# Kernel optimization log

Measured on AMD Instinct MI355X. Metric: run time of the kernel, lower is better.

The kernel has to match this reference:

```python
import jax, jax.numpy as jnp
import numpy as np

VOCAB, EMBD, H1, H2, OUT = 100000, 128, 256, 128, 1
EPS = 1e-12

def _layernorm(x, g, b):
    mu = jnp.mean(x, axis=-1, keepdims=True)
    var = jnp.mean(jnp.square(x - mu), axis=-1, keepdims=True)
    return (x - mu) * jax.lax.rsqrt(var + EPS) * g + b

def setup_inputs() -> dict:
    key = jax.random.key(0)
    ks = jax.random.split(key, 10)
    B, S = 4096, 50
    return {
        "entity_ids": jax.random.randint(ks[0], (B, S), 0, VOCAB),
        "entity_length": jax.random.randint(ks[1], (B,), 0, S + 1),
        "emb_table": jax.random.normal(ks[2], (VOCAB, EMBD), jnp.float32),
        "ln1_g": jnp.ones((EMBD,), jnp.float32),
        "ln1_b": jnp.zeros((EMBD,), jnp.float32),
        "w1": jax.random.normal(ks[3], (EMBD, H1), jnp.float32) * (1.0 / np.sqrt(EMBD)),
        "b1": jnp.zeros((H1,), jnp.float32),
        "w2": jax.random.normal(ks[4], (H1, H2), jnp.float32) * (1.0 / np.sqrt(H1)),
        "b2": jnp.zeros((H2,), jnp.float32),
        "ln2_g": jnp.ones((H2,), jnp.float32),
        "ln2_b": jnp.zeros((H2,), jnp.float32),
        "fc_w": jax.random.normal(ks[5], (H2, OUT), jnp.float32) * (1.0 / np.sqrt(H2)),
        "fc_b": jnp.zeros((OUT,), jnp.float32),
    }

def reference(entity_ids, entity_length, emb_table, ln1_g, ln1_b, w1, b1, w2, b2, ln2_g, ln2_b, fc_w, fc_b):
    # embed: [B, S, EMBD]
    x = emb_table[entity_ids]
    x = _layernorm(x, ln1_g, ln1_b)
    # MLP (dropout is identity in eval); torch GELU default is exact erf form
    x = jax.nn.gelu(x @ w1 + b1, approximate=False) @ w2 + b2  # [B, S, H2]
    # ragged max-pool over first length positions (length 0 treated as 1)
    lengths = jnp.maximum(entity_length, 1)  # [B]
    S = x.shape[1]
    mask = jnp.arange(S)[None, :] < lengths[:, None]  # [B, S]
    x = jnp.max(jnp.where(mask[:, :, None], x, -jnp.inf), axis=1)  # [B, H2]
    x = _layernorm(x, ln2_g, ln2_b)
    return (x @ fc_w + fc_b).squeeze(-1)  # [B]
```

## Files before the change

### kernel.cpp

```cpp
#include <hip/hip_runtime.h>
#include <hip/hip_bf16.h>
#include <math.h>

typedef __attribute__((ext_vector_type(8))) _Float16 half8;
typedef __attribute__((ext_vector_type(4))) float f32x4;

#define EMBD 128
#define H1 256
#define H2 128
#define SLEN 50

__device__ __forceinline__ float gelu_exact(float h) {
    float ah = fabsf(h);
    float d  = fmaf(0.23163845f, ah, 1.0f);
    float t;
    asm("v_rcp_f32 %0, %1" : "=v"(t) : "v"(d));
    float p = fmaf(1.061405429f, t, -1.453152027f);
    p = fmaf(p, t, 1.421413741f);
    p = fmaf(p, t, -0.284496736f);
    p = fmaf(p, t, 0.254829592f);
    p = p * t;
    float e;
    float x2 = h * h * -0.72134752f;
    asm("v_exp_f32 %0, %1" : "=v"(e) : "v"(x2));
    float er = fmaf(-p, e, 1.0f);
    return fmaf(0.5f * ah, er, 0.5f * h);
}

#define BARRIER_LDS() asm volatile("s_waitcnt lgkmcnt(0)\n\ts_barrier" ::: "memory")

__global__ __launch_bounds__(256) void prep_weights(
    const float* __restrict__ w1, const float* __restrict__ w2,
    half8* __restrict__ ws)
{
    int f = blockIdx.x * 256 + threadIdx.x;
    half8 v;
    if (f < 4096) {
        int lane = f & 63;
        int nt = (f >> 6) & 3, kt = (f >> 8) & 3, w = (f >> 10) & 3;
        int col = w * 64 + nt * 16 + (lane & 15);
        int kb  = kt * 32 + (lane >> 4) * 8;
        #pragma unroll
        for (int i = 0; i < 8; ++i) v[i] = (_Float16)w1[(size_t)(kb + i) * H1 + col];
        ws[f] = v;
    } else {
        int f2 = f - 4096;
        int lane = f2 & 63;
        int nt = (f2 >> 6) & 1, kt = (f2 >> 7) & 7, w = (f2 >> 10) & 3;
        int col = w * 32 + nt * 16 + (lane & 15);
        int kb  = kt * 32 + (lane >> 4) * 8;
        #pragma unroll
        for (int i = 0; i < 8; ++i) v[i] = (_Float16)w2[(size_t)(kb + i) * H2 + col];
        ws[4096 + f2] = v;
    }
}

__global__ __launch_bounds__(256, 2) void entity_encoder_kernel(
    const int* __restrict__ ids, const int* __restrict__ lens,
    const float* __restrict__ emb, const float* __restrict__ ln1g,
    const float* __restrict__ ln1b, const float* __restrict__ b1,
    const float* __restrict__ b2, const float* __restrict__ ln2g,
    const float* __restrict__ ln2b, const float* __restrict__ fcw,
    const float* __restrict__ fcb, const half8* __restrict__ wfrag,
    float* __restrict__ out)
{
    const int tid = threadIdx.x;
    const int w  = tid >> 6;
    const int l  = tid & 63;
    const int ln = l & 15;
    const int lg = l >> 4;
    const int g16 = w * 4 + lg;

    __shared__ __align__(16) _Float16 x_lds[32][EMBD + 8];
    __shared__ __align__(16) _Float16 h1_lds[32][H1 + 8];
    __shared__ float pool_lds[2][H2];

    half8 w1f[4][4];
    #pragma unroll
    for (int kt = 0; kt < 4; ++kt)
      #pragma unroll
      for (int nt = 0; nt < 4; ++nt)
        w1f[kt][nt] = wfrag[((w * 4 + kt) * 4 + nt) * 64 + l];
    half8 w2f[8][2];
    #pragma unroll
    for (int kt = 0; kt < 8; ++kt)
      #pragma unroll
      for (int nt = 0; nt < 2; ++nt)
        w2f[kt][nt] = wfrag[4096 + ((w * 8 + kt) * 2 + nt) * 64 + l];

    float g1r[8], b1r[8];
    #pragma unroll
    for (int i = 0; i < 8; ++i) { g1r[i] = ln1g[ln * 8 + i]; b1r[i] = ln1b[ln * 8 + i]; }
    float b1v[4];
    #pragma unroll
    for (int nt = 0; nt < 4; ++nt) b1v[nt] = b1[w * 64 + nt * 16 + ln];
    float b2v[2];
    #pragma unroll
    for (int nt = 0; nt < 2; ++nt) b2v[nt] = b2[w * 32 + nt * 16 + ln];
    float g2a = ln2g[l], g2c = ln2g[l + 64];
    float b2a = ln2b[l], b2c = ln2b[l + 64];
    float fwa = fcw[l],  fwc = fcw[l + 64];
    float fcb0 = fcb[0];

    int rows[4], Ts[4];
    #pragma unroll
    for (int i = 0; i < 4; ++i) {
        rows[i] = blockIdx.x + i * (int)gridDim.x;
        int T = lens[rows[i]];
        Ts[i] = T < 1 ? 1 : (T > SLEN ? SLEN : T);
    }

    float4 pa0[2], pa1[2]; bool va[2];
    #pragma unroll
    for (int s = 0; s < 2; ++s) {
        va[s] = (g16 < Ts[s]);
        if (va[s]) {
            int id = ids[rows[s] * SLEN + g16];
            const float4* src = (const float4*)(emb + (size_t)id * EMBD + ln * 8);
            pa0[s] = src[0]; pa1[s] = src[1];
        }
    }

    for (int j = 0; j < 2; ++j) {
        const int TA = Ts[2 * j], TB = Ts[2 * j + 1];
        const int ntA = (TA + 15) >> 4, ntB = (TB + 15) >> 4;
        const int ntiles = ntA > ntB ? ntA : ntB;
        float poolr[2][2];
        #pragma unroll
        for (int m = 0; m < 2; ++m) { poolr[m][0] = -INFINITY; poolr[m][1] = -INFINITY; }

        for (int mt = 0; mt < ntiles; ++mt) {
            #pragma unroll
            for (int s = 0; s < 2; ++s) {
                half8 xo;
                if (va[s]) {
                    float v[8] = {pa0[s].x, pa0[s].y, pa0[s].z, pa0[s].w,
                                  pa1[s].x, pa1[s].y, pa1[s].z, pa1[s].w};
                    float sm = 0.f, ss = 0.f;
                    #pragma unroll
                    for (int k = 0; k < 8; ++k) { sm += v[k]; ss += v[k] * v[k]; }
                    #pragma unroll
                    for (int m = 1; m < 16; m <<= 1) {
                        sm += __shfl_xor(sm, m, 64);
                        ss += __shfl_xor(ss, m, 64);
                    }
                    float mu  = sm * (1.f / 128.f);
                    float var = ss * (1.f / 128.f) - mu * mu;
                    float rs  = rsqrtf(var + 1e-12f);
                    #pragma unroll
                    for (int k = 0; k < 8; ++k)
                        xo[k] = (_Float16)((v[k] - mu) * rs * g1r[k] + b1r[k]);
                } else {
                    #pragma unroll
                    for (int k = 0; k < 8; ++k) xo[k] = (_Float16)0.f;
                }
                *(half8*)&x_lds[s * 16 + g16][ln * 8] = xo;
            }

            float4 pb0[2], pb1[2]; bool vb[2] = {false, false};
            {
                int nj = j, nmt = mt + 1;
                if (nmt >= ntiles) { nj = j + 1; nmt = 0; }
                if (nj < 2) {
                    #pragma unroll
                    for (int s = 0; s < 2; ++s) {
                        int tn = nmt * 16 + g16;
                        if (tn < Ts[2 * nj + s]) {
                            vb[s] = true;
                            int id = ids[rows[2 * nj + s] * SLEN + tn];
                            const float4* src = (const float4*)(emb + (size_t)id * EMBD + ln * 8);
                            pb0[s] = src[0]; pb1[s] = src[1];
                        }
                    }
                }
            }

            BARRIER_LDS();

            f32x4 acc[2][4];
            #pragma unroll
            for (int m = 0; m < 2; ++m)
              #pragma unroll
              for (int nt = 0; nt < 4; ++nt) acc[m][nt] = (f32x4){0,0,0,0};
            #pragma unroll
            for (int kt = 0; kt < 4; ++kt) {
                half8 a0 = *(const half8*)&x_lds[ln][kt * 32 + lg * 8];
                half8 a1 = *(const half8*)&x_lds[16 + ln][kt * 32 + lg * 8];
                #pragma unroll
                for (int nt = 0; nt < 4; ++nt) {
                    acc[0][nt] = __builtin_amdgcn_mfma_f32_16x16x32_f16(a0, w1f[kt][nt], acc[0][nt], 0, 0, 0);
                    acc[1][nt] = __builtin_amdgcn_mfma_f32_16x16x32_f16(a1, w1f[kt][nt], acc[1][nt], 0, 0, 0);
                }
            }
            #pragma unroll
            for (int m = 0; m < 2; ++m)
              #pragma unroll
              for (int nt = 0; nt < 4; ++nt) {
                int col = w * 64 + nt * 16 + ln;
                #pragma unroll
                for (int g2 = 0; g2 < 4; ++g2) {
                    int row = m * 16 + lg * 4 + g2;
                    float h = acc[m][nt][g2] + b1v[nt];
                    h1_lds[row][col] = (_Float16)gelu_exact(h);
                }
              }

            BARRIER_LDS();

            f32x4 acc2[2][2];
            #pragma unroll
            for (int m = 0; m < 2; ++m) { acc2[m][0] = (f32x4){0,0,0,0}; acc2[m][1] = (f32x4){0,0,0,0}; }
            #pragma unroll
            for (int kt = 0; kt < 8; ++kt) {
                half8 a0 = *(const half8*)&h1_lds[ln][kt * 32 + lg * 8];
                half8 a1 = *(const half8*)&h1_lds[16 + ln][kt * 32 + lg * 8];
                #pragma unroll
                for (int nt = 0; nt < 2; ++nt) {
                    acc2[0][nt] = __builtin_amdgcn_mfma_f32_16x16x32_f16(a0, w2f[kt][nt], acc2[0][nt], 0, 0, 0);
                    acc2[1][nt] = __builtin_amdgcn_mfma_f32_16x16x32_f16(a1, w2f[kt][nt], acc2[1][nt], 0, 0, 0);
                }
            }
            #pragma unroll
            for (int m = 0; m < 2; ++m) {
                const int Tm = m ? TB : TA;
                #pragma unroll
                for (int nt = 0; nt < 2; ++nt) {
                    float tm = -INFINITY;
                    #pragma unroll
                    for (int g2 = 0; g2 < 4; ++g2) {
                        int trow = lg * 4 + g2;
                        bool valid = (mt * 16 + trow) < Tm;
                        float h = acc2[m][nt][g2] + b2v[nt];
                        if (valid) tm = fmaxf(tm, h);
                    }
                    tm = fmaxf(tm, __shfl_xor(tm, 16, 64));
                    tm = fmaxf(tm, __shfl_xor(tm, 32, 64));
                    poolr[m][nt] = fmaxf(poolr[m][nt], tm);
                }
            }

            #pragma unroll
            for (int s = 0; s < 2; ++s) {
                if (vb[s]) { pa0[s] = pb0[s]; pa1[s] = pb1[s]; }
                va[s] = vb[s];
            }
        }

        if (lg == 0) {
            #pragma unroll
            for (int m = 0; m < 2; ++m)
              #pragma unroll
              for (int nt = 0; nt < 2; ++nt)
                pool_lds[m][w * 32 + nt * 16 + ln] = poolr[m][nt];
        }
        BARRIER_LDS();

        if (w < 2) {
            float v0 = pool_lds[w][l], v1 = pool_lds[w][l + 64];
            float s = v0 + v1, ss = v0 * v0 + v1 * v1;
            #pragma unroll
            for (int m = 1; m < 64; m <<= 1) {
                s  += __shfl_xor(s,  m, 64);
                ss += __shfl_xor(ss, m, 64);
            }
            float mu  = s * (1.f / 128.f);
            float var = ss * (1.f / 128.f) - mu * mu;
            float rs  = rsqrtf(var + 1e-12f);
            float n0 = (v0 - mu) * rs * g2a + b2a;
            float n1 = (v1 - mu) * rs * g2c + b2c;
            float dot = n0 * fwa + n1 * fwc;
            #pragma unroll
            for (int m = 1; m < 64; m <<= 1) dot += __shfl_xor(dot, m, 64);
            if (l == 0) out[rows[2 * j + w]] = dot + fcb0;
        }
        BARRIER_LDS();
    }
}

extern "C" void kernel_launch(void* const* d_in, const int* in_sizes, int n_in,
                              void* d_out, int out_size, void* d_ws, size_t ws_size,
                              hipStream_t stream) {
    const int*   ids  = (const int*)d_in[0];
    const int*   lens = (const int*)d_in[1];
    const float* emb  = (const float*)d_in[2];
    const float* ln1g = (const float*)d_in[3];
    const float* ln1b = (const float*)d_in[4];
    const float* w1   = (const float*)d_in[5];
    const float* b1   = (const float*)d_in[6];
    const float* w2   = (const float*)d_in[7];
    const float* b2   = (const float*)d_in[8];
    const float* ln2g = (const float*)d_in[9];
    const float* ln2b = (const float*)d_in[10];
    const float* fcw  = (const float*)d_in[11];
    const float* fcb  = (const float*)d_in[12];
    float* out = (float*)d_out;
    half8* ws = (half8*)d_ws;

    hipLaunchKernelGGL(prep_weights, dim3(32), dim3(256), 0, stream, w1, w2, ws);

    int nblocks = out_size / 4;
    hipLaunchKernelGGL(entity_encoder_kernel, dim3(nblocks), dim3(256), 0, stream,
                       ids, lens, emb, ln1g, ln1b, b1, b2, ln2g, ln2b, fcw, fcb,
                       ws, out);
}
```

Measured before the change: 79.86 us.

## Compact valid tokens into dense tiles and pool via segmented max with partials

Replaces the per-row padded tiling with a compaction pass that packs only the valid tokens (id plus row tag) into a dense stream. A persistent dense kernel processes full 32-token tiles, and a head kernel finishes the pooling and the final layernorm/fc. The aim is to remove wasted MFMA work on padding in partially filled 16-token tiles and to balance load across blocks. In exchange it adds three kernel launches, an atomic prefix step, a large partial-buffer initialisation, and segmented-max bookkeeping that relies on a row spanning at most three tiles.

```diff
diff --git a/kernel.cpp b/kernel.cpp
--- a/kernel.cpp
+++ b/kernel.cpp
@@ -3,12 +3,23 @@
 #include <math.h>
 
 typedef __attribute__((ext_vector_type(8))) _Float16 half8;
+typedef __attribute__((ext_vector_type(4))) _Float16 half4;
 typedef __attribute__((ext_vector_type(4))) float f32x4;
 
 #define EMBD 128
 #define H1 256
 #define H2 128
 #define SLEN 50
+#define NROWS 4096
+#define MAXTOK (NROWS * SLEN)
+#define MTILE 32
+#define MAXTILES ((MAXTOK + MTILE - 1) / MTILE)
+#define DENSE_GRID 1024
+
+#define WS_FRAGS   0
+#define WS_CNT     131072
+#define WS_PACKED  131200
+#define WS_PARTIAL 950400
 
 __device__ __forceinline__ float gelu_exact(float h) {
     float ah = fabsf(h);
@@ -29,40 +40,73 @@
 
 #define BARRIER_LDS() asm volatile("s_waitcnt lgkmcnt(0)\n\ts_barrier" ::: "memory")
 
-__global__ __launch_bounds__(256) void prep_weights(
+__global__ __launch_bounds__(256) void prep_kernel(
     const float* __restrict__ w1, const float* __restrict__ w2,
-    half8* __restrict__ ws)
+    half8* __restrict__ frags, int* __restrict__ cnt,
+    float* __restrict__ partial)
 {
-    int f = blockIdx.x * 256 + threadIdx.x;
-    half8 v;
-    if (f < 4096) {
-        int lane = f & 63;
-        int nt = (f >> 6) & 3, kt = (f >> 8) & 3, w = (f >> 10) & 3;
-        int col = w * 64 + nt * 16 + (lane & 15);
-        int kb  = kt * 32 + (lane >> 4) * 8;
-        #pragma unroll
-        for (int i = 0; i < 8; ++i) v[i] = (_Float16)w1[(size_t)(kb + i) * H1 + col];
-        ws[f] = v;
+    int b = blockIdx.x, t = threadIdx.x;
+    if (b < 32) {
+        int f = b * 256 + t;
+        half8 v;
+        if (f < 4096) {
+            int lane = f & 63;
+            int nt = (f >> 6) & 3, kt = (f >> 8) & 3, w = (f >> 10) & 3;
+            int col = w * 64 + nt * 16 + (lane & 15);
+            int kb  = kt * 32 + (lane >> 4) * 8;
+            #pragma unroll
+            for (int i = 0; i < 8; ++i) v[i] = (_Float16)w1[(size_t)(kb + i) * H1 + col];
+            frags[f] = v;
+        } else {
+            int f2 = f - 4096;
+            int lane = f2 & 63;
+            int nt = (f2 >> 6) & 1, kt = (f2 >> 7) & 7, w = (f2 >> 10) & 3;
+            int col = w * 32 + nt * 16 + (lane & 15);
+            int kb  = kt * 32 + (lane >> 4) * 8;
+            #pragma unroll
+            for (int i = 0; i < 8; ++i) v[i] = (_Float16)w2[(size_t)(kb + i) * H2 + col];
+            frags[4096 + f2] = v;
+        }
+    } else if (b == 32) {
+        if (t == 0) *cnt = 0;
     } else {
-        int f2 = f - 4096;
-        int lane = f2 & 63;
-        int nt = (f2 >> 6) & 1, kt = (f2 >> 7) & 7, w = (f2 >> 10) & 3;
-        int col = w * 32 + nt * 16 + (lane & 15);
-        int kb  = kt * 32 + (lane >> 4) * 8;
-        #pragma unroll
-        for (int i = 0; i < 8; ++i) v[i] = (_Float16)w2[(size_t)(kb + i) * H2 + col];
-        ws[4096 + f2] = v;
+        int idx = (b - 33) * 256 + t;
+        if (idx < NROWS * 256) {
+            int r = idx >> 8, rem = idx & 255;
+            partial[(size_t)r * 384 + 128 + rem] = -INFINITY;
+        }
     }
 }
 
-__global__ __launch_bounds__(256, 2) void entity_encoder_kernel(
+__global__ __launch_bounds__(256) void compact_kernel(
     const int* __restrict__ ids, const int* __restrict__ lens,
+    unsigned* __restrict__ packed, int* __restrict__ cnt)
+{
+    int gtid = blockIdx.x * 256 + threadIdx.x;
+    int lane = threadIdx.x & 63;
+    int len = lens[gtid]; len = len < 1 ? 1 : (len > SLEN ? SLEN : len);
+    int inc = len;
+    #pragma unroll
+    for (int off = 1; off < 64; off <<= 1) {
+        int v = __shfl_up(inc, off, 64);
+        if (lane >= off) inc += v;
+    }
+    int wave_total = __shfl(inc, 63, 64);
+    int wbase;
+    if (lane == 0) wbase = atomicAdd(cnt, wave_total);
+    wbase = __shfl(wbase, 0, 64);
+    int base = wbase + inc - len;
+    unsigned rtag = (unsigned)gtid << 17;
+    for (int t = 0; t < len; ++t)
+        packed[base + t] = (unsigned)ids[gtid * SLEN + t] | rtag;
+}
+
+__global__ __launch_bounds__(256) void dense_kernel(
+    const unsigned* __restrict__ packed, const int* __restrict__ cnt,
     const float* __restrict__ emb, const float* __restrict__ ln1g,
     const float* __restrict__ ln1b, const float* __restrict__ b1,
-    const float* __restrict__ b2, const float* __restrict__ ln2g,
-    const float* __restrict__ ln2b, const float* __restrict__ fcw,
-    const float* __restrict__ fcb, const half8* __restrict__ wfrag,
-    float* __restrict__ out)
+    const float* __restrict__ b2, const half8* __restrict__ wfrag,
+    float* __restrict__ partial)
 {
     const int tid = threadIdx.x;
     const int w  = tid >> 6;
@@ -71,9 +115,9 @@
     const int lg = l >> 4;
     const int g16 = w * 4 + lg;
 
-    __shared__ __align__(16) _Float16 x_lds[32][EMBD + 8];
-    __shared__ __align__(16) _Float16 h1_lds[32][H1 + 8];
-    __shared__ float pool_lds[2][H2];
+    __shared__ __align__(16) _Float16 x_lds[MTILE][EMBD + 8];
+    __shared__ __align__(16) _Float16 h1_lds[MTILE][H1 + 8];
+    __shared__ unsigned tok_lds[MTILE + 2];
 
     half8 w1f[4][4];
     #pragma unroll
@@ -91,190 +135,182 @@
     float g1r[8], b1r[8];
     #pragma unroll
     for (int i = 0; i < 8; ++i) { g1r[i] = ln1g[ln * 8 + i]; b1r[i] = ln1b[ln * 8 + i]; }
-    float b1v[4];
-    #pragma unroll
-    for (int nt = 0; nt < 4; ++nt) b1v[nt] = b1[w * 64 + nt * 16 + ln];
+    f32x4 b1tv[4];
+    #pragma unroll
+    for (int nt = 0; nt < 4; ++nt)
+        b1tv[nt] = *(const f32x4*)&b1[w * 64 + nt * 16 + lg * 4];
     float b2v[2];
     #pragma unroll
     for (int nt = 0; nt < 2; ++nt) b2v[nt] = b2[w * 32 + nt * 16 + ln];
+
+    const int total = *cnt;
+
+    for (int tile = blockIdx.x; tile * MTILE < total; tile += gridDim.x) {
+        const int base = tile * MTILE;
+
+        if (tid < MTILE) {
+            unsigned pk = 0xFFFFFFFFu;
+            if (base + tid < total) pk = packed[base + tid];
+            tok_lds[tid] = pk;
+        } else if (tid == MTILE) {
+            tok_lds[MTILE] = (base > 0) ? packed[base - 1] : 0xFFFFFFFFu;
+        }
+
+        #pragma unroll
+        for (int s = 0; s < 2; ++s) {
+            int tl = s * 16 + g16;
+            int gidx = base + tl;
+            half8 xo;
+            if (gidx < total) {
+                unsigned pk = packed[gidx];
+                int id = (int)(pk & 0x1FFFFu);
+                const float4* src = (const float4*)(emb + (size_t)id * EMBD + ln * 8);
+                float4 p0 = src[0], p1 = src[1];
+                float v[8] = {p0.x, p0.y, p0.z, p0.w, p1.x, p1.y, p1.z, p1.w};
+                float sm = 0.f, ss = 0.f;
+                #pragma unroll
+                for (int k = 0; k < 8; ++k) { sm += v[k]; ss += v[k] * v[k]; }
+                #pragma unroll
+                for (int m = 1; m < 16; m <<= 1) {
+                    sm += __shfl_xor(sm, m, 64);
+                    ss += __shfl_xor(ss, m, 64);
+                }
+                float mu  = sm * (1.f / 128.f);
+                float var = ss * (1.f / 128.f) - mu * mu;
+                float rs  = rsqrtf(var + 1e-12f);
+                #pragma unroll
+                for (int k = 0; k < 8; ++k)
+                    xo[k] = (_Float16)((v[k] - mu) * rs * g1r[k] + b1r[k]);
+            } else {
+                #pragma unroll
+                for (int k = 0; k < 8; ++k) xo[k] = (_Float16)0.f;
+            }
+            *(half8*)&x_lds[tl][ln * 8] = xo;
+        }
+
+        BARRIER_LDS();
+
+        f32x4 acc[2][4];
+        #pragma unroll
+        for (int m = 0; m < 2; ++m)
+          #pragma unroll
+          for (int nt = 0; nt < 4; ++nt) acc[m][nt] = (f32x4){0,0,0,0};
+        #pragma unroll
+        for (int kt = 0; kt < 4; ++kt) {
+            half8 bf0 = *(const half8*)&x_lds[ln][kt * 32 + lg * 8];
+            half8 bf1 = *(const half8*)&x_lds[16 + ln][kt * 32 + lg * 8];
+            #pragma unroll
+            for (int nt = 0; nt < 4; ++nt) {
+                acc[0][nt] = __builtin_amdgcn_mfma_f32_16x16x32_f16(w1f[kt][nt], bf0, acc[0][nt], 0, 0, 0);
+                acc[1][nt] = __builtin_amdgcn_mfma_f32_16x16x32_f16(w1f[kt][nt], bf1, acc[1][nt], 0, 0, 0);
+            }
+        }
+        #pragma unroll
+        for (int m = 0; m < 2; ++m)
+          #pragma unroll
+          for (int nt = 0; nt < 4; ++nt) {
+            half4 hv;
+            #pragma unroll
+            for (int g2 = 0; g2 < 4; ++g2) {
+                float h = acc[m][nt][g2] + b1tv[nt][g2];
+                hv[g2] = (_Float16)gelu_exact(h);
+            }
+            *(half4*)&h1_lds[m * 16 + ln][w * 64 + nt * 16 + lg * 4] = hv;
+          }
+
+        BARRIER_LDS();
+
+        f32x4 acc2[2][2];
+        #pragma unroll
+        for (int m = 0; m < 2; ++m) { acc2[m][0] = (f32x4){0,0,0,0}; acc2[m][1] = (f32x4){0,0,0,0}; }
+        #pragma unroll
+        for (int kt = 0; kt < 8; ++kt) {
+            half8 a0 = *(const half8*)&h1_lds[ln][kt * 32 + lg * 8];
+            half8 a1 = *(const half8*)&h1_lds[16 + ln][kt * 32 + lg * 8];
+            #pragma unroll
+            for (int nt = 0; nt < 2; ++nt) {
+                acc2[0][nt] = __builtin_amdgcn_mfma_f32_16x16x32_f16(a0, w2f[kt][nt], acc2[0][nt], 0, 0, 0);
+                acc2[1][nt] = __builtin_amdgcn_mfma_f32_16x16x32_f16(a1, w2f[kt][nt], acc2[1][nt], 0, 0, 0);
+            }
+        }
+        float val0[2][4], val1[2][4];
+        #pragma unroll
+        for (int m = 0; m < 2; ++m)
+          #pragma unroll
+          for (int g2 = 0; g2 < 4; ++g2) {
+            val0[m][g2] = acc2[m][0][g2] + b2v[0];
+            val1[m][g2] = acc2[m][1][g2] + b2v[1];
+          }
+
+        {
+            int prev_row = (int)(tok_lds[MTILE] >> 17);
+            int cur_row  = (int)(tok_lds[0] >> 17);
+            int s0 = 0;
+            bool firstSeg = true;
+            for (int j = 1; j <= MTILE; ++j) {
+                int rj = (j < MTILE) ? (int)(tok_lds[j] >> 17) : -1;
+                if (j == MTILE || rj != cur_row) {
+                    if (cur_row < NROWS) {
+                        float mx0 = -INFINITY, mx1 = -INFINITY;
+                        #pragma unroll
+                        for (int m = 0; m < 2; ++m)
+                          #pragma unroll
+                          for (int g2 = 0; g2 < 4; ++g2) {
+                            int tt = m * 16 + lg * 4 + g2;
+                            bool in = (tt >= s0) && (tt < j);
+                            if (in) { mx0 = fmaxf(mx0, val0[m][g2]); mx1 = fmaxf(mx1, val1[m][g2]); }
+                          }
+                        mx0 = fmaxf(mx0, __shfl_xor(mx0, 16, 64));
+                        mx0 = fmaxf(mx0, __shfl_xor(mx0, 32, 64));
+                        mx1 = fmaxf(mx1, __shfl_xor(mx1, 16, 64));
+                        mx1 = fmaxf(mx1, __shfl_xor(mx1, 32, 64));
+                        int side = 0;
+                        if (firstSeg && s0 == 0 && base > 0 && prev_row == cur_row)
+                            side = 1 + (tile & 1);
+                        if (lg == 0) {
+                            float* dst = partial + (size_t)cur_row * 384 + side * 128 + w * 32 + ln;
+                            dst[0]  = mx0;
+                            dst[16] = mx1;
+                        }
+                    }
+                    firstSeg = false;
+                    s0 = j; cur_row = rj;
+                }
+            }
+        }
+
+        BARRIER_LDS();
+    }
+}
+
+__global__ __launch_bounds__(256) void head_kernel(
+    const float* __restrict__ partial, const float* __restrict__ ln2g,
+    const float* __restrict__ ln2b, const float* __restrict__ fcw,
+    const float* __restrict__ fcb, float* __restrict__ out)
+{
+    int w = threadIdx.x >> 6, l = threadIdx.x & 63;
+    int r = blockIdx.x * 4 + w;
+    const float* pr = partial + (size_t)r * 384;
+    float v0 = fmaxf(fmaxf(pr[l],      pr[128 + l]),      pr[256 + l]);
+    float v1 = fmaxf(fmaxf(pr[64 + l], pr[128 + 64 + l]), pr[256 + 64 + l]);
     float g2a = ln2g[l], g2c = ln2g[l + 64];
     float b2a = ln2b[l], b2c = ln2b[l + 64];
     float fwa = fcw[l],  fwc = fcw[l + 64];
-    float fcb0 = fcb[0];
-
-    int rows[4], Ts[4];
-    #pragma unroll
-    for (int i = 0; i < 4; ++i) {
-        rows[i] = blockIdx.x + i * (int)gridDim.x;
-        int T = lens[rows[i]];
-        Ts[i] = T < 1 ? 1 : (T > SLEN ? SLEN : T);
+    float s = v0 + v1, ss = v0 * v0 + v1 * v1;
+    #pragma unroll
+    for (int m = 1; m < 64; m <<= 1) {
+        s  += __shfl_xor(s,  m, 64);
+        ss += __shfl_xor(ss, m, 64);
     }
-
-    float4 pa0[2], pa1[2]; bool va[2];
-    #pragma unroll
-    for (int s = 0; s < 2; ++s) {
-        va[s] = (g16 < Ts[s]);
-        if (va[s]) {
-            int id = ids[rows[s] * SLEN + g16];
-            const float4* src = (const float4*)(emb + (size_t)id * EMBD + ln * 8);
-            pa0[s] = src[0]; pa1[s] = src[1];
-        }
-    }
-
-    for (int j = 0; j < 2; ++j) {
-        const int TA = Ts[2 * j], TB = Ts[2 * j + 1];
-        const int ntA = (TA + 15) >> 4, ntB = (TB + 15) >> 4;
-        const int ntiles = ntA > ntB ? ntA : ntB;
-        float poolr[2][2];
-        #pragma unroll
-        for (int m = 0; m < 2; ++m) { poolr[m][0] = -INFINITY; poolr[m][1] = -INFINITY; }
-
-        for (int mt = 0; mt < ntiles; ++mt) {
-            #pragma unroll
-            for (int s = 0; s < 2; ++s) {
-                half8 xo;
-                if (va[s]) {
-                    float v[8] = {pa0[s].x, pa0[s].y, pa0[s].z, pa0[s].w,
-                                  pa1[s].x, pa1[s].y, pa1[s].z, pa1[s].w};
-                    float sm = 0.f, ss = 0.f;
-                    #pragma unroll
-                    for (int k = 0; k < 8; ++k) { sm += v[k]; ss += v[k] * v[k]; }
-                    #pragma unroll
-                    for (int m = 1; m < 16; m <<= 1) {
-                        sm += __shfl_xor(sm, m, 64);
-                        ss += __shfl_xor(ss, m, 64);
-                    }
-                    float mu  = sm * (1.f / 128.f);
-                    float var = ss * (1.f / 128.f) - mu * mu;
-                    float rs  = rsqrtf(var + 1e-12f);
-                    #pragma unroll
-                    for (int k = 0; k < 8; ++k)
-                        xo[k] = (_Float16)((v[k] - mu) * rs * g1r[k] + b1r[k]);
-                } else {
-                    #pragma unroll
-                    for (int k = 0; k < 8; ++k) xo[k] = (_Float16)0.f;
-                }
-                *(half8*)&x_lds[s * 16 + g16][ln * 8] = xo;
-            }
-
-            float4 pb0[2], pb1[2]; bool vb[2] = {false, false};
-            {
-                int nj = j, nmt = mt + 1;
-                if (nmt >= ntiles) { nj = j + 1; nmt = 0; }
-                if (nj < 2) {
-                    #pragma unroll
-                    for (int s = 0; s < 2; ++s) {
-                        int tn = nmt * 16 + g16;
-                        if (tn < Ts[2 * nj + s]) {
-                            vb[s] = true;
-                            int id = ids[rows[2 * nj + s] * SLEN + tn];
-                            const float4* src = (const float4*)(emb + (size_t)id * EMBD + ln * 8);
-                            pb0[s] = src[0]; pb1[s] = src[1];
-                        }
-                    }
-                }
-            }
-
-            BARRIER_LDS();
-
-            f32x4 acc[2][4];
-            #pragma unroll
-            for (int m = 0; m < 2; ++m)
-              #pragma unroll
-              for (int nt = 0; nt < 4; ++nt) acc[m][nt] = (f32x4){0,0,0,0};
-            #pragma unroll
-            for (int kt = 0; kt < 4; ++kt) {
-                half8 a0 = *(const half8*)&x_lds[ln][kt * 32 + lg * 8];
-                half8 a1 = *(const half8*)&x_lds[16 + ln][kt * 32 + lg * 8];
-                #pragma unroll
-                for (int nt = 0; nt < 4; ++nt) {
-                    acc[0][nt] = __builtin_amdgcn_mfma_f32_16x16x32_f16(a0, w1f[kt][nt], acc[0][nt], 0, 0, 0);
-                    acc[1][nt] = __builtin_amdgcn_mfma_f32_16x16x32_f16(a1, w1f[kt][nt], acc[1][nt], 0, 0, 0);
-                }
-            }
-            #pragma unroll
-            for (int m = 0; m < 2; ++m)
-              #pragma unroll
-              for (int nt = 0; nt < 4; ++nt) {
-                int col = w * 64 + nt * 16 + ln;
-                #pragma unroll
-                for (int g2 = 0; g2 < 4; ++g2) {
-                    int row = m * 16 + lg * 4 + g2;
-                    float h = acc[m][nt][g2] + b1v[nt];
-                    h1_lds[row][col] = (_Float16)gelu_exact(h);
-                }
-              }
-
-            BARRIER_LDS();
-
-            f32x4 acc2[2][2];
-            #pragma unroll
-            for (int m = 0; m < 2; ++m) { acc2[m][0] = (f32x4){0,0,0,0}; acc2[m][1] = (f32x4){0,0,0,0}; }
-            #pragma unroll
-            for (int kt = 0; kt < 8; ++kt) {
-                half8 a0 = *(const half8*)&h1_lds[ln][kt * 32 + lg * 8];
-                half8 a1 = *(const half8*)&h1_lds[16 + ln][kt * 32 + lg * 8];
-                #pragma unroll
-                for (int nt = 0; nt < 2; ++nt) {
-                    acc2[0][nt] = __builtin_amdgcn_mfma_f32_16x16x32_f16(a0, w2f[kt][nt], acc2[0][nt], 0, 0, 0);
-                    acc2[1][nt] = __builtin_amdgcn_mfma_f32_16x16x32_f16(a1, w2f[kt][nt], acc2[1][nt], 0, 0, 0);
-                }
-            }
-            #pragma unroll
-            for (int m = 0; m < 2; ++m) {
-                const int Tm = m ? TB : TA;
-                #pragma unroll
-                for (int nt = 0; nt < 2; ++nt) {
-                    float tm = -INFINITY;
-                    #pragma unroll
-                    for (int g2 = 0; g2 < 4; ++g2) {
-                        int trow = lg * 4 + g2;
-                        bool valid = (mt * 16 + trow) < Tm;
-                        float h = acc2[m][nt][g2] + b2v[nt];
-                        if (valid) tm = fmaxf(tm, h);
-                    }
-                    tm = fmaxf(tm, __shfl_xor(tm, 16, 64));
-                    tm = fmaxf(tm, __shfl_xor(tm, 32, 64));
-                    poolr[m][nt] = fmaxf(poolr[m][nt], tm);
-                }
-            }
-
-            #pragma unroll
-            for (int s = 0; s < 2; ++s) {
-                if (vb[s]) { pa0[s] = pb0[s]; pa1[s] = pb1[s]; }
-                va[s] = vb[s];
-            }
-        }
-
-        if (lg == 0) {
-            #pragma unroll
-            for (int m = 0; m < 2; ++m)
-              #pragma unroll
-              for (int nt = 0; nt < 2; ++nt)
-                pool_lds[m][w * 32 + nt * 16 + ln] = poolr[m][nt];
-        }
-        BARRIER_LDS();
-
-        if (w < 2) {
-            float v0 = pool_lds[w][l], v1 = pool_lds[w][l + 64];
-            float s = v0 + v1, ss = v0 * v0 + v1 * v1;
-            #pragma unroll
-            for (int m = 1; m < 64; m <<= 1) {
-                s  += __shfl_xor(s,  m, 64);
-                ss += __shfl_xor(ss, m, 64);
-            }
-            float mu  = s * (1.f / 128.f);
-            float var = ss * (1.f / 128.f) - mu * mu;
-            float rs  = rsqrtf(var + 1e-12f);
-            float n0 = (v0 - mu) * rs * g2a + b2a;
-            float n1 = (v1 - mu) * rs * g2c + b2c;
-            float dot = n0 * fwa + n1 * fwc;
-            #pragma unroll
-            for (int m = 1; m < 64; m <<= 1) dot += __shfl_xor(dot, m, 64);
-            if (l == 0) out[rows[2 * j + w]] = dot + fcb0;
-        }
-        BARRIER_LDS();
-    }
+    float mu  = s * (1.f / 128.f);
+    float var = ss * (1.f / 128.f) - mu * mu;
+    float rs  = rsqrtf(var + 1e-12f);
+    float n0 = (v0 - mu) * rs * g2a + b2a;
+    float n1 = (v1 - mu) * rs * g2c + b2c;
+    float dot = n0 * fwa + n1 * fwc;
+    #pragma unroll
+    for (int m = 1; m < 64; m <<= 1) dot += __shfl_xor(dot, m, 64);
+    if (l == 0) out[r] = dot + fcb[0];
 }
 
 extern "C" void kernel_launch(void* const* d_in, const int* in_sizes, int n_in,
@@ -294,12 +330,19 @@
     const float* fcw  = (const float*)d_in[11];
     const float* fcb  = (const float*)d_in[12];
     float* out = (float*)d_out;
-    half8* ws = (half8*)d_ws;
-
-    hipLaunchKernelGGL(prep_weights, dim3(32), dim3(256), 0, stream, w1, w2, ws);
-
-    int nblocks = out_size / 4;
-    hipLaunchKernelGGL(entity_encoder_kernel, dim3(nblocks), dim3(256), 0, stream,
-                       ids, lens, emb, ln1g, ln1b, b1, b2, ln2g, ln2b, fcw, fcb,
-                       ws, out);
-}
+
+    char* ws = (char*)d_ws;
+    half8*    frags   = (half8*)(ws + WS_FRAGS);
+    int*      cnt     = (int*)(ws + WS_CNT);
+    unsigned* packed  = (unsigned*)(ws + WS_PACKED);
+    float*    partial = (float*)(ws + WS_PARTIAL);
+
+    hipLaunchKernelGGL(prep_kernel, dim3(4129), dim3(256), 0, stream,
+                       w1, w2, frags, cnt, partial);
+    hipLaunchKernelGGL(compact_kernel, dim3(16), dim3(256), 0, stream,
+                       ids, lens, packed, cnt);
+    hipLaunchKernelGGL(dense_kernel, dim3(DENSE_GRID), dim3(256), 0, stream,
+                       packed, cnt, emb, ln1g, ln1b, b1, b2, frags, partial);
+    hipLaunchKernelGGL(head_kernel, dim3(1024), dim3(256), 0, stream,
+                       partial, ln2g, ln2b, fcw, fcb, out);
+}
```

After: 116.7 us. +46.1%, slower.
